# Kernel optimization log

Hardware: AMD Instinct MI355X
Metric: run time of the kernel (lower is better)

The kernel has to match this reference:

```python
import jax, jax.numpy as jnp
import numpy as np

# tcnn HashGrid config (from encoding_config)
L = 16          # n_levels
F = 2           # n_features_per_level
LOG2_T = 19     # log2_hashmap_size
T = 1 << LOG2_T
BASE_RES = 16.0
PER_LEVEL_SCALE = 1.3819
N_DIMS = 4

_PRIMES = np.array([1, 2654435761, 805459861, 3674653429], dtype=np.uint32)
# 16 corner offsets of the 4D hypercube, [16, 4] in {0,1}
_OFFSETS = ((np.arange(1 << N_DIMS)[:, None] >> np.arange(N_DIMS)[None, :]) & 1).astype(np.int32)


def hash_grid_encode(x, table):
    """x: [P, 4] in ~[0,1]; table: [L, T, F] -> [P, L*F]."""
    levels = jnp.arange(L, dtype=x.dtype)
    scales = jnp.exp2(levels * np.float32(np.log2(PER_LEVEL_SCALE))) * np.float32(BASE_RES) - 1.0  # [L]
    pos = x[:, None, :] * scales[None, :, None] + 0.5        # [P, L, 4]
    idxf = jnp.floor(pos)
    frac = pos - idxf                                        # [P, L, 4]
    idx = idxf.astype(jnp.int32)

    P = x.shape[0]
    h = jnp.zeros((P, L, 1 << N_DIMS), dtype=jnp.uint32)     # hashed corner indices
    w = jnp.ones((P, L, 1 << N_DIMS), dtype=x.dtype)         # quadrilinear weights
    for d in range(N_DIMS):  # small fixed loop over 4 dims
        off_d = _OFFSETS[None, None, :, d]                   # [1,1,16]
        coord = (idx[..., d:d + 1] + off_d).astype(jnp.uint32)
        h = h ^ (coord * jnp.uint32(_PRIMES[d]))
        fd = frac[..., d:d + 1]
        w = w * jnp.where(off_d == 1, fd, 1.0 - fd)
    h = (h & jnp.uint32(T - 1)).astype(jnp.int32)            # [P, L, 16]

    # gather per-level corner features: [P, L, 16, F]
    vals = table[jnp.arange(L)[None, :, None], h]
    feat = jnp.sum(w[..., None] * vals, axis=2)              # [P, L, F]
    return feat.reshape(P, L * F)


def setup_inputs() -> dict:
    key = jax.random.key(0)
    ks = jax.random.split(key, 9)
    B, N = 8, 32768
    inputs = jax.random.uniform(ks[0], (B, N, 3), dtype=jnp.float32)
    latent = jax.random.uniform(ks[1], (B, 1), dtype=jnp.float32)
    # hash table (tcnn inits uniform in [-1e-4, 1e-4])
    table = jax.random.uniform(ks[2], (L, T, F), jnp.float32, -1e-4, 1e-4)
    def lin(k, fan_in, fan_out):
        bound = 1.0 / np.sqrt(fan_in)
        kw, kb = jax.random.split(k)
        W = jax.random.uniform(kw, (fan_in, fan_out), jnp.float32, -bound, bound)
        b = jax.random.uniform(kb, (fan_out,), jnp.float32, -bound, bound)
        return W, b
    W1, b1 = lin(ks[3], 32, 64)
    W2, b2 = lin(ks[4], 64, 64)
    W3, b3 = lin(ks[5], 64, 3)
    return {"inputs": inputs, "latent": latent, "table": table,
            "W1": W1, "b1": b1, "W2": W2, "b2": b2, "W3": W3, "b3": b3}


def reference(inputs, latent, table, W1, b1, W2, b2, W3, b3):
    B, N, _ = inputs.shape
    inputs_con = jnp.broadcast_to(latent[:, None, :], (B, N, latent.shape[-1]))
    x = jnp.concatenate([inputs, inputs_con], axis=-1)       # [B, N, 4]
    x = (x + 1.0) / 2.0
    x = x.reshape(-1, N_DIMS)
    enc = hash_grid_encode(x, table)                         # [P, 32]
    h1 = jax.nn.gelu(enc @ W1 + b1, approximate=False)
    h2 = jax.nn.gelu(h1 @ W2 + b2, approximate=False)
    color = h2 @ W3 + b3                                     # [P, 3]
    return color.reshape(B, N, 3)
```

## Files before the change

### kernel.cpp

```cpp
#include <hip/hip_runtime.h>
#include <math.h>


#define NLEV 16
#define TSIZE (1u << 19)
#define TMASK (TSIZE - 1u)
#define NXCD 8

typedef __attribute__((ext_vector_type(8))) short bf16x8;
typedef __attribute__((ext_vector_type(4))) float f32x4;

union U32x4 { unsigned u[4]; uint4 q; bf16x8 v; };

__device__ __forceinline__ unsigned bfr(float x) {
    unsigned u = __float_as_uint(x);
    return (u + 0x7FFFu + ((u >> 16) & 1u)) >> 16;
}

__device__ __forceinline__ float gelu_fast(float x) {
    float ax = fabsf(x) * 0.70710678118654752440f;
    float t  = __builtin_amdgcn_rcpf(fmaf(0.3275911f, ax, 1.0f));
    float p  = t * (0.254829592f + t * (-0.284496736f + t * (1.421413741f +
               t * (-1.453152027f + t * 1.061405429f))));
    float e  = __expf(-ax * ax);
    float er = fmaf(-p, e, 1.0f);
    er = copysignf(er, x);
    return 0.5f * x * (1.0f + er);
}

__device__ __forceinline__ float gelu_exact(float x) {
    return 0.5f * x * (1.0f + erff(x * 0.70710678118654752440f));
}

__global__ __launch_bounds__(256, 6) void ngp_encode(
    const float* __restrict__ inputs,
    const float* __restrict__ latent,
    const float* __restrict__ table,
    unsigned* __restrict__ encb,
    int P, int bplShift, int nShift)
{
    const int bid = blockIdx.x;
    const int xcd = bid & (NXCD - 1);
    const int j   = bid >> 3;
    const int l   = xcd * (NLEV / NXCD) + (j >> bplShift);
    const int p   = ((j & ((1 << bplShift) - 1)) << 8) + threadIdx.x;

    float x0 = inputs[p * 3 + 0];
    float x1 = inputs[p * 3 + 1];
    float x2 = inputs[p * 3 + 2];
    float x3 = latent[p >> nShift];
    x0 = (x0 + 1.0f) * 0.5f;
    x1 = (x1 + 1.0f) * 0.5f;
    x2 = (x2 + 1.0f) * 0.5f;
    x3 = (x3 + 1.0f) * 0.5f;

    const float LOG2S = (float)log2(1.3819);
    const float s = exp2f((float)l * LOG2S) * 16.0f - 1.0f;

    const float px = fmaf(x0, s, 0.5f);
    const float py = fmaf(x1, s, 0.5f);
    const float pz = fmaf(x2, s, 0.5f);
    const float pw = fmaf(x3, s, 0.5f);
    const float fx = floorf(px), fy = floorf(py), fz = floorf(pz), fw = floorf(pw);
    const float rx = px - fx, ry = py - fy, rz = pz - fz, rw = pw - fw;

    const unsigned a0 = (unsigned)(int)fx;               const unsigned a1 = a0 + 1u;
    const unsigned b0 = (unsigned)(int)fy * 2654435761u; const unsigned b1v = b0 + 2654435761u;
    const unsigned c0 = (unsigned)(int)fz * 805459861u;  const unsigned c1 = c0 + 805459861u;
    const unsigned d0 = (unsigned)(int)fw * 3674653429u; const unsigned d1 = d0 + 3674653429u;

    const float wx0 = 1.0f - rx, wy0 = 1.0f - ry, wz0 = 1.0f - rz, ww0 = 1.0f - rw;
    const float wzw[4] = { wz0 * ww0, rz * ww0, wz0 * rw, rz * rw };

    const float2* __restrict__ tab2 = (const float2*)table + (unsigned)l * TSIZE;

    float acc0 = 0.0f, acc1 = 0.0f;

    if ((a0 & 1u) == 0u) {
        #pragma unroll
        for (int t = 0; t < 8; ++t) {
            const unsigned rest = ((t & 1) ? b1v : b0) ^ ((t & 2) ? c1 : c0)
                                ^ ((t & 4) ? d1 : d0);
            const float wrest = ((t & 1) ? ry : wy0) * wzw[t >> 1];
            const unsigned i0 = (a0 ^ rest) & TMASK;
            const float4 q = *(const float4*)(tab2 + (i0 & ~1u));
            const bool lowIs0 = (i0 & 1u) == 0u;
            const float v0x = lowIs0 ? q.x : q.z;
            const float v0y = lowIs0 ? q.y : q.w;
            const float v1x = lowIs0 ? q.z : q.x;
            const float v1y = lowIs0 ? q.w : q.y;
            const float we = wx0 * wrest;
            const float wo = rx  * wrest;
            acc0 = fmaf(we, v0x, fmaf(wo, v1x, acc0));
            acc1 = fmaf(we, v0y, fmaf(wo, v1y, acc1));
        }
    } else {
        #pragma unroll
        for (int t = 0; t < 8; ++t) {
            const unsigned rest = ((t & 1) ? b1v : b0) ^ ((t & 2) ? c1 : c0)
                                ^ ((t & 4) ? d1 : d0);
            const float wrest = ((t & 1) ? ry : wy0) * wzw[t >> 1];
            const float2 v0 = tab2[(a0 ^ rest) & TMASK];
            const float2 v1 = tab2[(a1 ^ rest) & TMASK];
            const float we = wx0 * wrest;
            const float wo = rx  * wrest;
            acc0 = fmaf(we, v0.x, fmaf(wo, v1.x, acc0));
            acc1 = fmaf(we, v0.y, fmaf(wo, v1.y, acc1));
        }
    }
    __builtin_nontemporal_store(bfr(acc0) | (bfr(acc1) << 16), &encb[l * P + p]);
}

__global__ __launch_bounds__(256) void ngp_mlp_mfma(
    const unsigned* __restrict__ encb,
    const float* __restrict__ W1, const float* __restrict__ b1,
    const float* __restrict__ W2, const float* __restrict__ b2,
    const float* __restrict__ W3, const float* __restrict__ b3,
    float* __restrict__ out, int P)
{
    __shared__ __align__(16) unsigned char sH[4 * 8192];

    const int tid  = threadIdx.x;
    const int w    = tid >> 6;
    const int lane = tid & 63;
    const int lo16 = lane & 15;
    const int hi4  = lane >> 4;
    const int pbase = blockIdx.x * 256 + w * 64;
    char* const myH = (char*)sH + w * 8192;

    bf16x8 w1f[4];
    #pragma unroll
    for (int mt = 0; mt < 4; ++mt) {
        const int m = mt * 16 + lo16;
        const int kg = hi4 * 8;
        bf16x8 f;
        #pragma unroll
        for (int j = 0; j < 4; ++j) {
            f[2 * j    ] = (short)bfr(W1[(kg + 2 * j    ) * 64 + m]);
            f[2 * j + 1] = (short)bfr(W1[(kg + 2 * j + 1) * 64 + m]);
        }
        w1f[mt] = f;
    }
    bf16x8 w2f[4][2];
    #pragma unroll
    for (int mt = 0; mt < 4; ++mt) {
        const int m = mt * 16 + lo16;
        #pragma unroll
        for (int kc = 0; kc < 2; ++kc) {
            const int kg = kc * 32 + hi4 * 8;
            bf16x8 f;
            #pragma unroll
            for (int j = 0; j < 4; ++j) {
                f[2 * j    ] = (short)bfr(W2[(kg + 2 * j    ) * 64 + m]);
                f[2 * j + 1] = (short)bfr(W2[(kg + 2 * j + 1) * 64 + m]);
            }
            w2f[mt][kc] = f;
        }
    }
    bf16x8 w3f[2];
    {
        const int m = (lo16 < 3) ? lo16 : 2;
        #pragma unroll
        for (int kc = 0; kc < 2; ++kc) {
            const int kg = kc * 32 + hi4 * 8;
            bf16x8 f;
            #pragma unroll
            for (int j = 0; j < 4; ++j) {
                f[2 * j    ] = (short)bfr(W3[(kg + 2 * j    ) * 3 + m]);
                f[2 * j + 1] = (short)bfr(W3[(kg + 2 * j + 1) * 3 + m]);
            }
            w3f[kc] = f;
        }
    }

    const f32x4 zero = {0.0f, 0.0f, 0.0f, 0.0f};

    f32x4 acc1[4][4];
    #pragma unroll
    for (int mt = 0; mt < 4; ++mt)
        #pragma unroll
        for (int nt = 0; nt < 4; ++nt) acc1[mt][nt] = zero;

    #pragma unroll
    for (int nt = 0; nt < 4; ++nt) {
        const int p = pbase + nt * 16 + lo16;
        const int lev0 = hi4 * 4;
        U32x4 bu;
        #pragma unroll
        for (int j = 0; j < 4; ++j) bu.u[j] = encb[(lev0 + j) * P + p];
        #pragma unroll
        for (int mt = 0; mt < 4; ++mt)
            acc1[mt][nt] = __builtin_amdgcn_mfma_f32_16x16x32_bf16(
                w1f[mt], bu.v, acc1[mt][nt], 0, 0, 0);
    }

    float4 b1v[4];
    #pragma unroll
    for (int mt = 0; mt < 4; ++mt)
        b1v[mt] = *(const float4*)(b1 + mt * 16 + hi4 * 4);

    #pragma unroll
    for (int mt = 0; mt < 4; ++mt) {
        const int nb  = mt * 16 + hi4 * 4;
        const int blkb = nb >> 3;
        #pragma unroll
        for (int nt = 0; nt < 4; ++nt) {
            const f32x4 a = acc1[mt][nt];
            const float h0 = gelu_fast(a[0] + b1v[mt].x);
            const float h1 = gelu_fast(a[1] + b1v[mt].y);
            const float h2 = gelu_fast(a[2] + b1v[mt].z);
            const float h3 = gelu_fast(a[3] + b1v[mt].w);
            const int pl = nt * 16 + lo16;
            char* dst = myH + pl * 128 + ((blkb ^ (pl & 7)) * 16) + ((nb & 7) * 2);
            *(uint2*)dst = make_uint2(bfr(h0) | (bfr(h1) << 16),
                                      bfr(h2) | (bfr(h3) << 16));
        }
    }

    f32x4 acc2[4][4];
    #pragma unroll
    for (int mt = 0; mt < 4; ++mt)
        #pragma unroll
        for (int nt = 0; nt < 4; ++nt) acc2[mt][nt] = zero;

    #pragma unroll
    for (int kc = 0; kc < 2; ++kc) {
        #pragma unroll
        for (int nt = 0; nt < 4; ++nt) {
            const int pl = nt * 16 + lo16;
            const int kb = kc * 4 + hi4;
            const char* src = myH + pl * 128 + ((kb ^ (pl & 7)) * 16);
            U32x4 bu; bu.q = *(const uint4*)src;
            #pragma unroll
            for (int mt = 0; mt < 4; ++mt)
                acc2[mt][nt] = __builtin_amdgcn_mfma_f32_16x16x32_bf16(
                    w2f[mt][kc], bu.v, acc2[mt][nt], 0, 0, 0);
        }
    }

    float4 b2v[4];
    #pragma unroll
    for (int mt = 0; mt < 4; ++mt)
        b2v[mt] = *(const float4*)(b2 + mt * 16 + hi4 * 4);

    #pragma unroll
    for (int mt = 0; mt < 4; ++mt) {
        const int nb  = mt * 16 + hi4 * 4;
        const int blkb = nb >> 3;
        #pragma unroll
        for (int nt = 0; nt < 4; ++nt) {
            const f32x4 a = acc2[mt][nt];
            const float h0 = gelu_fast(a[0] + b2v[mt].x);
            const float h1 = gelu_fast(a[1] + b2v[mt].y);
            const float h2 = gelu_fast(a[2] + b2v[mt].z);
            const float h3 = gelu_fast(a[3] + b2v[mt].w);
            const int pl = nt * 16 + lo16;
            char* dst = myH + pl * 128 + ((blkb ^ (pl & 7)) * 16) + ((nb & 7) * 2);
            *(uint2*)dst = make_uint2(bfr(h0) | (bfr(h1) << 16),
                                      bfr(h2) | (bfr(h3) << 16));
        }
    }

    f32x4 acc3[4];
    #pragma unroll
    for (int nt = 0; nt < 4; ++nt) acc3[nt] = zero;

    #pragma unroll
    for (int kc = 0; kc < 2; ++kc) {
        #pragma unroll
        for (int nt = 0; nt < 4; ++nt) {
            const int pl = nt * 16 + lo16;
            const int kb = kc * 4 + hi4;
            const char* src = myH + pl * 128 + ((kb ^ (pl & 7)) * 16);
            U32x4 bu; bu.q = *(const uint4*)src;
            acc3[nt] = __builtin_amdgcn_mfma_f32_16x16x32_bf16(
                w3f[kc], bu.v, acc3[nt], 0, 0, 0);
        }
    }

    const float b30 = b3[0], b31 = b3[1], b32 = b3[2];
    if (hi4 == 0) {
        #pragma unroll
        for (int nt = 0; nt < 4; ++nt) {
            const int p = pbase + nt * 16 + lo16;
            out[p * 3 + 0] = acc3[nt][0] + b30;
            out[p * 3 + 1] = acc3[nt][1] + b31;
            out[p * 3 + 2] = acc3[nt][2] + b32;
        }
    }
}

__global__ __launch_bounds__(256) void ngp_fused(
    const float* __restrict__ inputs, const float* __restrict__ latent,
    const float* __restrict__ table,
    const float* __restrict__ W1, const float* __restrict__ b1,
    const float* __restrict__ W2, const float* __restrict__ b2,
    const float* __restrict__ W3, const float* __restrict__ b3,
    float* __restrict__ out)
{
    const int p = blockIdx.x * 256 + threadIdx.x;
    float x0 = inputs[p * 3 + 0];
    float x1 = inputs[p * 3 + 1];
    float x2 = inputs[p * 3 + 2];
    float x3 = latent[p >> 15];
    x0 = (x0 + 1.0f) * 0.5f; x1 = (x1 + 1.0f) * 0.5f;
    x2 = (x2 + 1.0f) * 0.5f; x3 = (x3 + 1.0f) * 0.5f;

    float h1[64];
    #pragma unroll
    for (int j = 0; j < 64; ++j) h1[j] = 0.0f;

    const float LOG2S = (float)log2(1.3819);
    const float2* __restrict__ tab2 = (const float2*)table;

    #pragma unroll 2
    for (int l = 0; l < NLEV; ++l) {
        const float s = exp2f((float)l * LOG2S) * 16.0f - 1.0f;
        const float px = fmaf(x0, s, 0.5f);
        const float py = fmaf(x1, s, 0.5f);
        const float pz = fmaf(x2, s, 0.5f);
        const float pw = fmaf(x3, s, 0.5f);
        const float fx = floorf(px), fy = floorf(py), fz = floorf(pz), fw = floorf(pw);
        const float rx = px - fx, ry = py - fy, rz = pz - fz, rw = pw - fw;
        const unsigned a0 = (unsigned)(int)fx;               const unsigned a1 = a0 + 1u;
        const unsigned b0 = (unsigned)(int)fy * 2654435761u; const unsigned b1v = b0 + 2654435761u;
        const unsigned c0 = (unsigned)(int)fz * 805459861u;  const unsigned c1 = c0 + 805459861u;
        const unsigned d0 = (unsigned)(int)fw * 3674653429u; const unsigned d1 = d0 + 3674653429u;
        const float wx0 = 1.0f - rx, wy0 = 1.0f - ry, wz0 = 1.0f - rz, ww0 = 1.0f - rw;
        const float wxy[4] = { wx0 * wy0, rx * wy0, wx0 * ry, rx * ry };
        const float wzw[4] = { wz0 * ww0, rz * ww0, wz0 * rw, rz * rw };
        const unsigned base = (unsigned)l * TSIZE;
        float acc0 = 0.0f, acc1 = 0.0f;
        #pragma unroll
        for (int c = 0; c < 16; ++c) {
            unsigned h = ((c & 1) ? a1 : a0) ^ ((c & 2) ? b1v : b0)
                       ^ ((c & 4) ? c1 : c0) ^ ((c & 8) ? d1 : d0);
            const float2 v = tab2[base + (h & TMASK)];
            const float wgt = wxy[c & 3] * wzw[c >> 2];
            acc0 = fmaf(wgt, v.x, acc0);
            acc1 = fmaf(wgt, v.y, acc1);
        }
        const float* __restrict__ w0 = W1 + (2 * l) * 64;
        const float* __restrict__ w1 = W1 + (2 * l + 1) * 64;
        #pragma unroll
        for (int j = 0; j < 64; ++j) {
            h1[j] = fmaf(acc0, w0[j], fmaf(acc1, w1[j], h1[j]));
        }
    }
    #pragma unroll
    for (int j = 0; j < 64; ++j) h1[j] = gelu_exact(h1[j] + b1[j]);

    float col0 = b3[0], col1 = b3[1], col2 = b3[2];
    #pragma unroll 1
    for (int ch = 0; ch < 8; ++ch) {
        float acc[8];
        #pragma unroll
        for (int k = 0; k < 8; ++k) acc[k] = b2[ch * 8 + k];
        #pragma unroll
        for (int i = 0; i < 64; ++i) {
            const float hv = h1[i];
            const float* __restrict__ wr = W2 + i * 64 + ch * 8;
            #pragma unroll
            for (int k = 0; k < 8; ++k) acc[k] = fmaf(hv, wr[k], acc[k]);
        }
        #pragma unroll
        for (int k = 0; k < 8; ++k) {
            const float g = gelu_exact(acc[k]);
            const int j2 = ch * 8 + k;
            col0 = fmaf(g, W3[j2 * 3 + 0], col0);
            col1 = fmaf(g, W3[j2 * 3 + 1], col1);
            col2 = fmaf(g, W3[j2 * 3 + 2], col2);
        }
    }
    out[p * 3 + 0] = col0;
    out[p * 3 + 1] = col1;
    out[p * 3 + 2] = col2;
}

extern "C" void kernel_launch(void* const* d_in, const int* in_sizes, int n_in,
                              void* d_out, int out_size, void* d_ws, size_t ws_size,
                              hipStream_t stream) {
    const float* inputs = (const float*)d_in[0];
    const float* latent = (const float*)d_in[1];
    const float* table  = (const float*)d_in[2];
    const float* W1 = (const float*)d_in[3];
    const float* b1 = (const float*)d_in[4];
    const float* W2 = (const float*)d_in[5];
    const float* b2 = (const float*)d_in[6];
    const float* W3 = (const float*)d_in[7];
    const float* b3 = (const float*)d_in[8];
    float* out = (float*)d_out;

    const int P = in_sizes[0] / 3;
    const int B = in_sizes[1];
    const int N = P / B;
    const int nShift = 31 - __builtin_clz(N);
    const int bpl = P / 256;
    const int bplShift = 31 - __builtin_clz(bpl);

    const size_t encBytes = (size_t)P * NLEV * sizeof(unsigned);
    const bool shapeOK = (P & 255) == 0 && (bpl & (bpl - 1)) == 0 &&
                         (N & (N - 1)) == 0 && bpl >= 8;

    if (shapeOK && ws_size >= encBytes) {
        unsigned* encb = (unsigned*)d_ws;
        ngp_encode<<<dim3(bpl * NLEV), dim3(256), 0, stream>>>(
            inputs, latent, table, encb, P, bplShift, nShift);
        ngp_mlp_mfma<<<dim3(P / 256), dim3(256), 0, stream>>>(
            encb, W1, b1, W2, b2, W3, b3, out, P);
    } else {
        ngp_fused<<<dim3(P / 256), dim3(256), 0, stream>>>(
            inputs, latent, table, W1, b1, W2, b2, W3, b3, out);
    }
}
```

Baseline: 203.7 us.

## Stage coarse hash-grid levels as dense bf16 tiles in LDS

After: 205.0 us. No clear change (+0.6%).

```diff
diff --git a/kernel.cpp b/kernel.cpp
--- a/kernel.cpp
+++ b/kernel.cpp
@@ -5,7 +5,6 @@
 #define NLEV 16
 #define TSIZE (1u << 19)
 #define TMASK (TSIZE - 1u)
-#define NXCD 8
 
 typedef __attribute__((ext_vector_type(8))) short bf16x8;
 typedef __attribute__((ext_vector_type(4))) float f32x4;
@@ -32,6 +31,85 @@
     return 0.5f * x * (1.0f + erff(x * 0.70710678118654752440f));
 }
 
+#define LOG2S_CONST ((float)log2(1.3819))
+
+__global__ __launch_bounds__(256) void ngp_encode_lds(
+    const float* __restrict__ inputs,
+    const float* __restrict__ latent,
+    const float* __restrict__ table,
+    unsigned* __restrict__ encb,
+    int P, int nShift)
+{
+    __shared__ unsigned sTab[18 * 18 * 18 * 2];
+
+    const int bid = blockIdx.x;
+    const int l   = bid >> 7;
+    const int blk = bid & 127;
+    const int pBase = blk * 2048;
+    const int D = (l == 0) ? 10 : (l == 1) ? 13 : 18;
+    const int E = D * D * D * 2;
+    const int sx = D * D * 2, sy = D * 2;
+
+    const float s = exp2f((float)l * LOG2S_CONST) * 16.0f - 1.0f;
+    const int bx = (int)floorf(fmaf(0.5f, s, 0.5f));
+
+    const float x3 = (latent[pBase >> nShift] + 1.0f) * 0.5f;
+    const float pw = fmaf(x3, s, 0.5f);
+    const float fw = floorf(pw);
+    const float rw = pw - fw;
+    const int   iw = (int)fw;
+    const float ww0 = 1.0f - rw;
+
+    const float2* __restrict__ tab2 = (const float2*)table + (unsigned)l * TSIZE;
+    for (int e = threadIdx.x; e < E; e += 256) {
+        const int lw = e & 1;
+        int r = e >> 1;
+        const int lz = r % D; r /= D;
+        const int ly = r % D;
+        const int lx = r / D;
+        const unsigned cx = (unsigned)(bx + lx);
+        const unsigned cy = (unsigned)(bx + ly);
+        const unsigned cz = (unsigned)(bx + lz);
+        const unsigned cw = (unsigned)(iw + lw);
+        const unsigned h = cx ^ cy * 2654435761u ^ cz * 805459861u ^ cw * 3674653429u;
+        const float2 v = tab2[h & TMASK];
+        sTab[e] = bfr(v.x) | (bfr(v.y) << 16);
+    }
+    __syncthreads();
+
+    for (int t = 0; t < 8; ++t) {
+        const int p = pBase + t * 256 + threadIdx.x;
+        const float x0 = (inputs[p * 3 + 0] + 1.0f) * 0.5f;
+        const float x1 = (inputs[p * 3 + 1] + 1.0f) * 0.5f;
+        const float x2 = (inputs[p * 3 + 2] + 1.0f) * 0.5f;
+        const float px = fmaf(x0, s, 0.5f);
+        const float py = fmaf(x1, s, 0.5f);
+        const float pz = fmaf(x2, s, 0.5f);
+        const float fx = floorf(px), fy = floorf(py), fz = floorf(pz);
+        const float rx = px - fx, ry = py - fy, rz = pz - fz;
+        const int lx = (int)fx - bx, ly = (int)fy - bx, lz = (int)fz - bx;
+
+        const float wx0 = 1.0f - rx, wy0 = 1.0f - ry, wz0 = 1.0f - rz;
+        const float wxy[4] = { wx0 * wy0, rx * wy0, wx0 * ry, rx * ry };
+        const float wzw[4] = { wz0 * ww0, rz * ww0, wz0 * rw, rz * rw };
+
+        const int base = lx * sx + ly * sy + lz * 2;
+        float acc0 = 0.0f, acc1 = 0.0f;
+        #pragma unroll
+        for (int c = 0; c < 16; ++c) {
+            const int idx = base + ((c & 1) ? sx : 0) + ((c & 2) ? sy : 0)
+                          + ((c & 4) ? 2 : 0) + (c >> 3);
+            const unsigned ev = sTab[idx];
+            const float v0 = __uint_as_float(ev << 16);
+            const float v1 = __uint_as_float(ev & 0xFFFF0000u);
+            const float wgt = wxy[c & 3] * wzw[c >> 2];
+            acc0 = fmaf(wgt, v0, acc0);
+            acc1 = fmaf(wgt, v1, acc1);
+        }
+        __builtin_nontemporal_store(bfr(acc0) | (bfr(acc1) << 16), &encb[l * P + p]);
+    }
+}
+
 __global__ __launch_bounds__(256, 6) void ngp_encode(
     const float* __restrict__ inputs,
     const float* __restrict__ latent,
@@ -40,10 +118,8 @@
     int P, int bplShift, int nShift)
 {
     const int bid = blockIdx.x;
-    const int xcd = bid & (NXCD - 1);
-    const int j   = bid >> 3;
-    const int l   = xcd * (NLEV / NXCD) + (j >> bplShift);
-    const int p   = ((j & ((1 << bplShift) - 1)) << 8) + threadIdx.x;
+    const int l   = 3 + (bid >> bplShift);
+    const int p   = ((bid & ((1 << bplShift) - 1)) << 8) + threadIdx.x;
 
     float x0 = inputs[p * 3 + 0];
     float x1 = inputs[p * 3 + 1];
@@ -54,8 +130,7 @@
     x2 = (x2 + 1.0f) * 0.5f;
     x3 = (x3 + 1.0f) * 0.5f;
 
-    const float LOG2S = (float)log2(1.3819);
-    const float s = exp2f((float)l * LOG2S) * 16.0f - 1.0f;
+    const float s = exp2f((float)l * LOG2S_CONST) * 16.0f - 1.0f;
 
     const float px = fmaf(x0, s, 0.5f);
     const float py = fmaf(x1, s, 0.5f);
@@ -310,12 +385,11 @@
     #pragma unroll
     for (int j = 0; j < 64; ++j) h1[j] = 0.0f;
 
-    const float LOG2S = (float)log2(1.3819);
     const float2* __restrict__ tab2 = (const float2*)table;
 
     #pragma unroll 2
     for (int l = 0; l < NLEV; ++l) {
-        const float s = exp2f((float)l * LOG2S) * 16.0f - 1.0f;
+        const float s = exp2f((float)l * LOG2S_CONST) * 16.0f - 1.0f;
         const float px = fmaf(x0, s, 0.5f);
         const float py = fmaf(x1, s, 0.5f);
         const float pz = fmaf(x2, s, 0.5f);
@@ -399,12 +473,14 @@
     const int bplShift = 31 - __builtin_clz(bpl);
 
     const size_t encBytes = (size_t)P * NLEV * sizeof(unsigned);
-    const bool shapeOK = (P & 255) == 0 && (bpl & (bpl - 1)) == 0 &&
-                         (N & (N - 1)) == 0 && bpl >= 8;
+    const bool shapeOK = (P & 2047) == 0 && (bpl & (bpl - 1)) == 0 &&
+                         (N & (N - 1)) == 0 && N >= 2048 && P / 2048 == 128;
 
     if (shapeOK && ws_size >= encBytes) {
         unsigned* encb = (unsigned*)d_ws;
-        ngp_encode<<<dim3(bpl * NLEV), dim3(256), 0, stream>>>(
+        ngp_encode_lds<<<dim3(3 * 128), dim3(256), 0, stream>>>(
+            inputs, latent, table, encb, P, nShift);
+        ngp_encode<<<dim3(bpl * 13), dim3(256), 0, stream>>>(
             inputs, latent, table, encb, P, bplShift, nShift);
         ngp_mlp_mfma<<<dim3(P / 256), dim3(256), 0, stream>>>(
             encb, W1, b1, W2, b2, W3, b3, out, P);
```
